# Performance work log

Hardware: AMD Instinct MI355X
Metric: run time of the kernel (lower is better)

## Reference

```python
import jax, jax.numpy as jnp
import numpy as np

NUM_STEPS = 8
THRESHOLD = 0.5


def _glorot(key, shape):
    fan_in = shape[0]
    return jax.random.normal(key, shape, dtype=jnp.float32) / np.sqrt(fan_in).astype(np.float32)


def setup_inputs() -> dict:
    key = jax.random.key(0)
    ks = jax.random.split(key, 24)
    B, APM = 2048, 32           # molecules, atoms per molecule
    N = B * APM                 # 65536 nodes
    E = N * 4                   # 262144 directed edges
    NF, EF, NH, EH, MA = 64, 16, 128, 128, 256
    inp = {}
    inp['mol_a_reprs'] = jax.random.normal(ks[0], (B, MA), dtype=jnp.float32)
    inp['node_features'] = jax.random.normal(ks[1], (N, NF), dtype=jnp.float32)
    inp['edge_features'] = jax.random.normal(ks[2], (E, EF), dtype=jnp.float32)
    inp['node_hidden0'] = jnp.zeros((N, NH), dtype=jnp.float32)
    inp['edge_hidden0'] = jnp.zeros((E, EH), dtype=jnp.float32)
    inp['edges'] = jax.random.randint(ks[3], (2, E), 0, N, dtype=jnp.int32)
    inp['batch_indices'] = jnp.repeat(jnp.arange(B, dtype=jnp.int32), APM)  # sorted, in-range
    # MPN weights (no bias)
    inp['W1'] = _glorot(ks[4], (NF, EH))   # src node features -> edge hidden
    inp['W2'] = _glorot(ks[5], (EF, EH))   # edge features -> edge hidden
    inp['W3'] = _glorot(ks[6], (NH, EH))   # src node hidden -> edge hidden
    inp['U1'] = _glorot(ks[7], (NF, NH))   # node features -> node hidden
    inp['U2'] = _glorot(ks[8], (EH, NH))   # aggregated edge hidden -> node hidden
    # pick-atom MLP: (MA+NH)->256->128->64->1
    inp['M1w'] = _glorot(ks[9], (MA + NH, 256)); inp['M1b'] = jnp.zeros((256,), jnp.float32)
    inp['M2w'] = _glorot(ks[10], (256, 128));    inp['M2b'] = jnp.zeros((128,), jnp.float32)
    inp['M3w'] = _glorot(ks[11], (128, 64));     inp['M3b'] = jnp.zeros((64,), jnp.float32)
    inp['M4w'] = _glorot(ks[12], (64, 1));       inp['M4b'] = jnp.zeros((1,), jnp.float32)
    return inp


def _mpn(node_features, edge_features, node_h, edge_h, src, dst, W1, W2, W3, U1, U2):
    N = node_features.shape[0]
    W1x_src = node_features[src] @ W1          # [E, EH], loop-invariant
    W2e = edge_features @ W2                   # [E, EH], loop-invariant
    U1x = node_features @ U1                   # [N, NH], loop-invariant
    for _ in range(NUM_STEPS):
        agg = jax.ops.segment_sum(edge_h, dst, num_segments=N)   # [N, EH]
        node_h = jax.nn.relu(U1x + agg @ U2)                     # [N, NH]
        edge_h = jax.nn.relu(W1x_src + W2e + node_h[src] @ W3)   # [E, EH]
    return node_h


def reference(mol_a_reprs, node_features, edge_features, node_hidden0, edge_hidden0,
              edges, batch_indices, W1, W2, W3, U1, U2,
              M1w, M1b, M2w, M2b, M3w, M3b, M4w, M4b):
    src, dst = edges[0], edges[1]
    node_h = _mpn(node_features, edge_features, node_hidden0, edge_hidden0,
                  src, dst, W1, W2, W3, U1, U2)
    b_atom_mol_a = mol_a_reprs[batch_indices]                    # index_select gather [N, MA]
    x = jnp.concatenate([node_h, b_atom_mol_a], axis=1)          # [N, NH+MA]
    x = jax.nn.relu(x @ M1w + M1b)
    x = jax.nn.relu(x @ M2w + M2b)
    x = jax.nn.relu(x @ M3w + M3b)
    p = jax.nn.sigmoid(x @ M4w + M4b)                            # [N, 1]
    return p >= THRESHOLD
```

## Files before the change

kernel.cpp:

```cpp
#include <hip/hip_runtime.h>
#include <cstddef>

#define NF 64
#define EF 16
#define NH 128
#define EH 128
#define MA 256

static inline int ceil_div(int a, int b) { return (a + b - 1) / b; }

__global__ __launch_bounds__(256) void gemm128_kernel(
    const float* __restrict__ A, const float* __restrict__ Bw,
    float* __restrict__ C,
    const float* __restrict__ addR, const int* __restrict__ addIdx,
    const float* __restrict__ bias, const int* __restrict__ gatherA,
    int M, int K, int Nc, int doRelu)
{
    __shared__ float As[16][132];
    __shared__ float Bs[16][132];
    const int tid = threadIdx.x;
    const int tx = tid & 15;
    const int ty = tid >> 4;
    const int m0 = blockIdx.y << 7;
    const int n0 = blockIdx.x << 7;

    const int lr = tid >> 1;
    const int lc = (tid & 1) << 3;
    const int br = tid >> 4;
    const int bc = (tid & 15) << 3;

    float acc[8][8];
#pragma unroll
    for (int i = 0; i < 8; ++i)
#pragma unroll
        for (int j = 0; j < 8; ++j) acc[i][j] = 0.0f;

    int arow = gatherA ? gatherA[m0 + lr] : (m0 + lr);
    const float* aptr = A + (size_t)arow * K + lc;

    for (int k0 = 0; k0 < K; k0 += 16) {
        float4 a0 = *(const float4*)(aptr + k0);
        float4 a1 = *(const float4*)(aptr + k0 + 4);
        float4 b0 = *(const float4*)(Bw + (size_t)(k0 + br) * Nc + n0 + bc);
        float4 b1 = *(const float4*)(Bw + (size_t)(k0 + br) * Nc + n0 + bc + 4);
        __syncthreads();
        As[lc + 0][lr] = a0.x; As[lc + 1][lr] = a0.y; As[lc + 2][lr] = a0.z; As[lc + 3][lr] = a0.w;
        As[lc + 4][lr] = a1.x; As[lc + 5][lr] = a1.y; As[lc + 6][lr] = a1.z; As[lc + 7][lr] = a1.w;
        *(float4*)&Bs[br][bc] = b0;
        *(float4*)&Bs[br][bc + 4] = b1;
        __syncthreads();
#pragma unroll
        for (int kk = 0; kk < 16; ++kk) {
            float4 av0 = *(const float4*)&As[kk][ty * 8];
            float4 av1 = *(const float4*)&As[kk][ty * 8 + 4];
            float4 bv0 = *(const float4*)&Bs[kk][tx * 8];
            float4 bv1 = *(const float4*)&Bs[kk][tx * 8 + 4];
            float a[8] = {av0.x, av0.y, av0.z, av0.w, av1.x, av1.y, av1.z, av1.w};
            float b[8] = {bv0.x, bv0.y, bv0.z, bv0.w, bv1.x, bv1.y, bv1.z, bv1.w};
#pragma unroll
            for (int i = 0; i < 8; ++i)
#pragma unroll
                for (int j = 0; j < 8; ++j)
                    acc[i][j] = fmaf(a[i], b[j], acc[i][j]);
        }
    }

    const int c = n0 + tx * 8;
    float4 bvl = make_float4(0.f, 0.f, 0.f, 0.f), bvh = bvl;
    if (bias) { bvl = *(const float4*)(bias + c); bvh = *(const float4*)(bias + c + 4); }
#pragma unroll
    for (int i = 0; i < 8; ++i) {
        int r = m0 + ty * 8 + i;
        float4 vl = make_float4(acc[i][0], acc[i][1], acc[i][2], acc[i][3]);
        float4 vh = make_float4(acc[i][4], acc[i][5], acc[i][6], acc[i][7]);
        if (addR) {
            int ar = addIdx ? addIdx[r] : r;
            float4 al = *(const float4*)(addR + (size_t)ar * Nc + c);
            float4 ah = *(const float4*)(addR + (size_t)ar * Nc + c + 4);
            vl.x += al.x; vl.y += al.y; vl.z += al.z; vl.w += al.w;
            vh.x += ah.x; vh.y += ah.y; vh.z += ah.z; vh.w += ah.w;
        }
        vl.x += bvl.x; vl.y += bvl.y; vl.z += bvl.z; vl.w += bvl.w;
        vh.x += bvh.x; vh.y += bvh.y; vh.z += bvh.z; vh.w += bvh.w;
        if (doRelu) {
            vl.x = fmaxf(vl.x, 0.f); vl.y = fmaxf(vl.y, 0.f); vl.z = fmaxf(vl.z, 0.f); vl.w = fmaxf(vl.w, 0.f);
            vh.x = fmaxf(vh.x, 0.f); vh.y = fmaxf(vh.y, 0.f); vh.z = fmaxf(vh.z, 0.f); vh.w = fmaxf(vh.w, 0.f);
        }
        *(float4*)(C + (size_t)r * Nc + c) = vl;
        *(float4*)(C + (size_t)r * Nc + c + 4) = vh;
    }
}

__global__ __launch_bounds__(256) void gemm_kernel(
    const float* __restrict__ A, const float* __restrict__ Bw,
    float* __restrict__ C,
    const float* __restrict__ addR, const int* __restrict__ addIdx,
    const float* __restrict__ bias,
    int M, int K, int Nc, int doRelu)
{
    __shared__ float As[16][64];
    __shared__ float Bs[16][64];
    const int tid = threadIdx.x;
    const int tx = tid & 15, ty = tid >> 4;
    const int m0 = blockIdx.y << 6;
    const int n0 = blockIdx.x << 6;
    const int lr = tid >> 2;
    const int lc = (tid & 3) << 2;
    const int bkr = tid >> 4;
    const int bc = (tid & 15) << 2;

    float acc[4][4];
#pragma unroll
    for (int i = 0; i < 4; ++i)
#pragma unroll
        for (int j = 0; j < 4; ++j) acc[i][j] = 0.0f;

    for (int k0 = 0; k0 < K; k0 += 16) {
        float4 a4 = *(const float4*)(A + (size_t)(m0 + lr) * K + (k0 + lc));
        float4 b4 = *(const float4*)(Bw + (size_t)(k0 + bkr) * Nc + (n0 + bc));
        __syncthreads();
        As[lc + 0][lr] = a4.x;
        As[lc + 1][lr] = a4.y;
        As[lc + 2][lr] = a4.z;
        As[lc + 3][lr] = a4.w;
        *(float4*)&Bs[bkr][bc] = b4;
        __syncthreads();
#pragma unroll
        for (int kk = 0; kk < 16; ++kk) {
            float a0 = As[kk][ty * 4 + 0];
            float a1 = As[kk][ty * 4 + 1];
            float a2 = As[kk][ty * 4 + 2];
            float a3 = As[kk][ty * 4 + 3];
            float b0 = Bs[kk][tx * 4 + 0];
            float b1 = Bs[kk][tx * 4 + 1];
            float b2 = Bs[kk][tx * 4 + 2];
            float b3 = Bs[kk][tx * 4 + 3];
            acc[0][0] += a0 * b0; acc[0][1] += a0 * b1; acc[0][2] += a0 * b2; acc[0][3] += a0 * b3;
            acc[1][0] += a1 * b0; acc[1][1] += a1 * b1; acc[1][2] += a1 * b2; acc[1][3] += a1 * b3;
            acc[2][0] += a2 * b0; acc[2][1] += a2 * b1; acc[2][2] += a2 * b2; acc[2][3] += a2 * b3;
            acc[3][0] += a3 * b0; acc[3][1] += a3 * b1; acc[3][2] += a3 * b2; acc[3][3] += a3 * b3;
        }
    }

    const int c = n0 + tx * 4;
    float4 bv = make_float4(0.f, 0.f, 0.f, 0.f);
    if (bias) bv = *(const float4*)(bias + c);
#pragma unroll
    for (int i = 0; i < 4; ++i) {
        int r = m0 + ty * 4 + i;
        float4 v = make_float4(acc[i][0], acc[i][1], acc[i][2], acc[i][3]);
        if (addR) {
            int ar = addIdx ? addIdx[r] : r;
            float4 ad = *(const float4*)(addR + (size_t)ar * Nc + c);
            v.x += ad.x; v.y += ad.y; v.z += ad.z; v.w += ad.w;
        }
        v.x += bv.x; v.y += bv.y; v.z += bv.z; v.w += bv.w;
        if (doRelu) {
            v.x = fmaxf(v.x, 0.f); v.y = fmaxf(v.y, 0.f);
            v.z = fmaxf(v.z, 0.f); v.w = fmaxf(v.w, 0.f);
        }
        *(float4*)(C + (size_t)r * Nc + c) = v;
    }
}

__global__ __launch_bounds__(256) void hist_kernel(const int* __restrict__ dst, int* __restrict__ deg, int E) {
    int e = blockIdx.x * 256 + threadIdx.x;
    if (e < E) atomicAdd(&deg[dst[e]], 1);
}

__global__ __launch_bounds__(256) void scan_block_kernel(const int* __restrict__ deg, int* __restrict__ rp,
                                                         int* __restrict__ bsum) {
    __shared__ int buf[256];
    int tid = threadIdx.x;
    int i = blockIdx.x * 256 + tid;
    int v = deg[i];
    buf[tid] = v;
    __syncthreads();
    for (int off = 1; off < 256; off <<= 1) {
        int t = (tid >= off) ? buf[tid - off] : 0;
        __syncthreads();
        buf[tid] += t;
        __syncthreads();
    }
    rp[i] = buf[tid] - v;
    if (tid == 255) bsum[blockIdx.x] = buf[255];
}

__global__ __launch_bounds__(256) void scan_top_kernel(const int* __restrict__ bsum, int* __restrict__ boff,
                                                       int* __restrict__ rp, int N) {
    __shared__ int buf[256];
    int tid = threadIdx.x;
    int v = bsum[tid];
    buf[tid] = v;
    __syncthreads();
    for (int off = 1; off < 256; off <<= 1) {
        int t = (tid >= off) ? buf[tid - off] : 0;
        __syncthreads();
        buf[tid] += t;
        __syncthreads();
    }
    boff[tid] = buf[tid] - v;
    if (tid == 255) rp[N] = buf[255];
}

__global__ __launch_bounds__(256) void scan_add_kernel(int* __restrict__ rp, int* __restrict__ cursor,
                                                       const int* __restrict__ boff) {
    int tid = threadIdx.x;
    int i = blockIdx.x * 256 + tid;
    int v = rp[i] + boff[blockIdx.x];
    rp[i] = v;
    cursor[i] = v;
}

__global__ __launch_bounds__(256) void scatter_kernel(const int* __restrict__ dst, const int* __restrict__ src,
                                                      int* __restrict__ cursor,
                                                      int* __restrict__ eid, int* __restrict__ srcS, int E) {
    int e = blockIdx.x * 256 + threadIdx.x;
    if (e < E) {
        int p = atomicAdd(&cursor[dst[e]], 1);
        eid[p] = e;
        srcS[p] = src[e];
    }
}

__global__ __launch_bounds__(256) void relu_copy_kernel(const float* __restrict__ in, float* __restrict__ out, int n4) {
    int i = blockIdx.x * 256 + threadIdx.x;
    if (i < n4) {
        float4 v = ((const float4*)in)[i];
        v.x = fmaxf(v.x, 0.f); v.y = fmaxf(v.y, 0.f);
        v.z = fmaxf(v.z, 0.f); v.w = fmaxf(v.w, 0.f);
        ((float4*)out)[i] = v;
    }
}

__global__ __launch_bounds__(128) void agg_kernel(const float* __restrict__ nodeT, const float* __restrict__ W2eS,
                                                  const int* __restrict__ rp, const int* __restrict__ srcS,
                                                  float* __restrict__ agg) {
    int n = blockIdx.x * 4 + threadIdx.y;
    int c = threadIdx.x << 2;
    int p0 = rp[n], p1 = rp[n + 1];
    float4 s = make_float4(0.f, 0.f, 0.f, 0.f);
    for (int p = p0; p < p1; ++p) {
        int sn = srcS[p];
        float4 t = *(const float4*)(nodeT + (size_t)sn * EH + c);
        float4 w = *(const float4*)(W2eS + (size_t)p * EH + c);
        s.x += fmaxf(t.x + w.x, 0.f);
        s.y += fmaxf(t.y + w.y, 0.f);
        s.z += fmaxf(t.z + w.z, 0.f);
        s.w += fmaxf(t.w + w.w, 0.f);
    }
    *(float4*)(agg + (size_t)n * EH + c) = s;
}

__global__ __launch_bounds__(256) void final_kernel(const float* __restrict__ x3, const float* __restrict__ w,
                                                    const float* __restrict__ b, int* __restrict__ out, int Nn) {
    int g = blockIdx.x * 256 + threadIdx.x;
    int n = g >> 6;
    int lane = threadIdx.x & 63;
    if (n < Nn) {
        float v = x3[(size_t)n * 64 + lane] * w[lane];
#pragma unroll
        for (int off = 32; off > 0; off >>= 1) v += __shfl_xor(v, off, 64);
        if (lane == 0) out[n] = (v + b[0]) >= 0.f ? 1 : 0;
    }
}

extern "C" void kernel_launch(void* const* d_in, const int* in_sizes, int n_in,
                              void* d_out, int out_size, void* d_ws, size_t ws_size,
                              hipStream_t stream)
{
    const float* mol_a = (const float*)d_in[0];
    const float* nf    = (const float*)d_in[1];
    const float* ef    = (const float*)d_in[2];
    const int*   edges = (const int*)d_in[5];
    const int*   batch = (const int*)d_in[6];
    const float* W1  = (const float*)d_in[7];
    const float* W2  = (const float*)d_in[8];
    const float* W3  = (const float*)d_in[9];
    const float* U1  = (const float*)d_in[10];
    const float* U2  = (const float*)d_in[11];
    const float* M1w = (const float*)d_in[12];
    const float* M1b = (const float*)d_in[13];
    const float* M2w = (const float*)d_in[14];
    const float* M2b = (const float*)d_in[15];
    const float* M3w = (const float*)d_in[16];
    const float* M3b = (const float*)d_in[17];
    const float* M4w = (const float*)d_in[18];
    const float* M4b = (const float*)d_in[19];

    const int N = in_sizes[3] / NH;
    const int E = in_sizes[4] / EH;
    const int B = in_sizes[0] / MA;
    const int* srcp = edges;
    const int* dstp = edges + E;

    char* ws = (char*)d_ws;
    size_t off = 0;
    auto alloc = [&](size_t bytes) -> char* {
        char* p = ws + off;
        off = (off + bytes + 255) & ~(size_t)255;
        return p;
    };
    int* deg     = (int*)alloc((size_t)N * 4);
    int* rp      = (int*)alloc(((size_t)N + 1) * 4);
    int* cursor  = (int*)alloc((size_t)N * 4);
    int* bsum    = (int*)alloc(256 * 4);
    int* boff    = (int*)alloc(256 * 4);
    int* eid     = (int*)alloc((size_t)E * 4);
    int* srcS    = (int*)alloc((size_t)E * 4);
    float* nodePre = (float*)alloc((size_t)N * EH * 4);
    float* U1x     = (float*)alloc((size_t)N * NH * 4);
    float* node_h  = (float*)alloc((size_t)N * NH * 4);
    float* nodeT   = (float*)alloc((size_t)N * EH * 4);
    float* aggp    = (float*)alloc((size_t)N * EH * 4);
    float* molPart = (float*)alloc((size_t)B * 256 * 4);
    float* W2eS    = (float*)alloc((size_t)E * EH * 4);
    float* x1 = (float*)W2eS;
    float* x2 = nodeT;
    float* x3 = aggp;

    hipMemsetAsync(deg, 0, (size_t)N * 4, stream);
    hist_kernel<<<ceil_div(E, 256), 256, 0, stream>>>(dstp, deg, E);
    scan_block_kernel<<<N / 256, 256, 0, stream>>>(deg, rp, bsum);
    scan_top_kernel<<<1, 256, 0, stream>>>(bsum, boff, rp, N);
    scan_add_kernel<<<N / 256, 256, 0, stream>>>(rp, cursor, boff);
    scatter_kernel<<<ceil_div(E, 256), 256, 0, stream>>>(dstp, srcp, cursor, eid, srcS, E);

    gemm128_kernel<<<dim3(1, N / 128), 256, 0, stream>>>(nf, W1, nodePre, nullptr, nullptr, nullptr, nullptr, N, NF, EH, 0);
    gemm128_kernel<<<dim3(1, E / 128), 256, 0, stream>>>(ef, W2, W2eS, nullptr, nullptr, nullptr, eid, E, EF, EH, 0);
    gemm128_kernel<<<dim3(1, N / 128), 256, 0, stream>>>(nf, U1, U1x, nullptr, nullptr, nullptr, nullptr, N, NF, NH, 0);

    relu_copy_kernel<<<(N * NH / 4) / 256, 256, 0, stream>>>(U1x, node_h, N * NH / 4);

    for (int s = 0; s < 7; ++s) {
        gemm128_kernel<<<dim3(1, N / 128), 256, 0, stream>>>(node_h, W3, nodeT, nodePre, nullptr, nullptr, nullptr, N, NH, EH, 0);
        agg_kernel<<<N / 4, dim3(32, 4), 0, stream>>>(nodeT, W2eS, rp, srcS, aggp);
        gemm128_kernel<<<dim3(1, N / 128), 256, 0, stream>>>(aggp, U2, node_h, U1x, nullptr, nullptr, nullptr, N, EH, NH, 1);
    }

    gemm_kernel<<<dim3(256 / 64, B / 64), 256, 0, stream>>>(mol_a, M1w + 128 * 256, molPart, nullptr, nullptr, M1b, B, MA, 256, 0);
    gemm128_kernel<<<dim3(2, N / 128), 256, 0, stream>>>(node_h, M1w, x1, molPart, batch, nullptr, nullptr, N, NH, 256, 1);
    gemm128_kernel<<<dim3(1, N / 128), 256, 0, stream>>>(x1, M2w, x2, nullptr, nullptr, M2b, nullptr, N, 256, 128, 1);
    gemm_kernel<<<dim3(1, N / 64), 256, 0, stream>>>(x2, M3w, x3, nullptr, nullptr, M3b, N, 128, 64, 1);
    final_kernel<<<ceil_div(N * 64, 256), 256, 0, stream>>>(x3, M4w, M4b, (int*)d_out, N);
}
```

Baseline: 1.387 ms.

## Fuse aggregation, U2 and W3 GEMMs into one per-step kernel and fuse MLP tail

```diff
diff --git a/kernel.cpp b/kernel.cpp
--- a/kernel.cpp
+++ b/kernel.cpp
@@ -14,7 +14,7 @@
     float* __restrict__ C,
     const float* __restrict__ addR, const int* __restrict__ addIdx,
     const float* __restrict__ bias, const int* __restrict__ gatherA,
-    int M, int K, int Nc, int doRelu)
+    int M, int K, int Nc, int doRelu, int reluA)
 {
     __shared__ float As[16][132];
     __shared__ float Bs[16][132];
@@ -43,6 +43,10 @@
         float4 a1 = *(const float4*)(aptr + k0 + 4);
         float4 b0 = *(const float4*)(Bw + (size_t)(k0 + br) * Nc + n0 + bc);
         float4 b1 = *(const float4*)(Bw + (size_t)(k0 + br) * Nc + n0 + bc + 4);
+        if (reluA) {
+            a0.x = fmaxf(a0.x, 0.f); a0.y = fmaxf(a0.y, 0.f); a0.z = fmaxf(a0.z, 0.f); a0.w = fmaxf(a0.w, 0.f);
+            a1.x = fmaxf(a1.x, 0.f); a1.y = fmaxf(a1.y, 0.f); a1.z = fmaxf(a1.z, 0.f); a1.w = fmaxf(a1.w, 0.f);
+        }
         __syncthreads();
         As[lc + 0][lr] = a0.x; As[lc + 1][lr] = a0.y; As[lc + 2][lr] = a0.z; As[lc + 3][lr] = a0.w;
         As[lc + 4][lr] = a1.x; As[lc + 5][lr] = a1.y; As[lc + 6][lr] = a1.z; As[lc + 7][lr] = a1.w;
@@ -91,75 +95,131 @@
     }
 }
 
-__global__ __launch_bounds__(256) void gemm_kernel(
-    const float* __restrict__ A, const float* __restrict__ Bw,
-    float* __restrict__ C,
-    const float* __restrict__ addR, const int* __restrict__ addIdx,
-    const float* __restrict__ bias,
-    int M, int K, int Nc, int doRelu)
+__global__ __launch_bounds__(256, 2) void fused_step_kernel(
+    const float* __restrict__ nodeT_in, const float* __restrict__ W2eS,
+    const int* __restrict__ rp, const int* __restrict__ srcS,
+    const float* __restrict__ U1x, const float* __restrict__ U2,
+    const float* __restrict__ nodePre, const float* __restrict__ W3,
+    float* __restrict__ nodeT_out, float* __restrict__ node_h_out,
+    int writeNodeH, int doGemm2)
 {
-    __shared__ float As[16][64];
-    __shared__ float Bs[16][64];
+    __shared__ float As[128][132];
+    __shared__ float Bs[16][132];
     const int tid = threadIdx.x;
+    const int m0 = blockIdx.x << 7;
+
+    {
+        const int cx = (tid & 31) << 2;
+        const int ry = tid >> 5;
+        for (int rg = 0; rg < 16; ++rg) {
+            const int row = rg * 8 + ry;
+            const int n = m0 + row;
+            const int p0 = rp[n], p1 = rp[n + 1];
+            float4 s = make_float4(0.f, 0.f, 0.f, 0.f);
+            for (int p = p0; p < p1; ++p) {
+                const int sn = srcS[p];
+                float4 t = *(const float4*)(nodeT_in + (size_t)sn * EH + cx);
+                float4 w = *(const float4*)(W2eS + (size_t)p * EH + cx);
+                s.x += fmaxf(t.x + w.x, 0.f);
+                s.y += fmaxf(t.y + w.y, 0.f);
+                s.z += fmaxf(t.z + w.z, 0.f);
+                s.w += fmaxf(t.w + w.w, 0.f);
+            }
+            As[cx + 0][row] = s.x;
+            As[cx + 1][row] = s.y;
+            As[cx + 2][row] = s.z;
+            As[cx + 3][row] = s.w;
+        }
+    }
+    __syncthreads();
+
     const int tx = tid & 15, ty = tid >> 4;
-    const int m0 = blockIdx.y << 6;
-    const int n0 = blockIdx.x << 6;
-    const int lr = tid >> 2;
-    const int lc = (tid & 3) << 2;
-    const int bkr = tid >> 4;
-    const int bc = (tid & 15) << 2;
-
-    float acc[4][4];
-#pragma unroll
-    for (int i = 0; i < 4; ++i)
-#pragma unroll
-        for (int j = 0; j < 4; ++j) acc[i][j] = 0.0f;
-
-    for (int k0 = 0; k0 < K; k0 += 16) {
-        float4 a4 = *(const float4*)(A + (size_t)(m0 + lr) * K + (k0 + lc));
-        float4 b4 = *(const float4*)(Bw + (size_t)(k0 + bkr) * Nc + (n0 + bc));
-        __syncthreads();
-        As[lc + 0][lr] = a4.x;
-        As[lc + 1][lr] = a4.y;
-        As[lc + 2][lr] = a4.z;
-        As[lc + 3][lr] = a4.w;
-        *(float4*)&Bs[bkr][bc] = b4;
-        __syncthreads();
-#pragma unroll
-        for (int kk = 0; kk < 16; ++kk) {
-            float a0 = As[kk][ty * 4 + 0];
-            float a1 = As[kk][ty * 4 + 1];
-            float a2 = As[kk][ty * 4 + 2];
-            float a3 = As[kk][ty * 4 + 3];
-            float b0 = Bs[kk][tx * 4 + 0];
-            float b1 = Bs[kk][tx * 4 + 1];
-            float b2 = Bs[kk][tx * 4 + 2];
-            float b3 = Bs[kk][tx * 4 + 3];
-            acc[0][0] += a0 * b0; acc[0][1] += a0 * b1; acc[0][2] += a0 * b2; acc[0][3] += a0 * b3;
-            acc[1][0] += a1 * b0; acc[1][1] += a1 * b1; acc[1][2] += a1 * b2; acc[1][3] += a1 * b3;
-            acc[2][0] += a2 * b0; acc[2][1] += a2 * b1; acc[2][2] += a2 * b2; acc[2][3] += a2 * b3;
-            acc[3][0] += a3 * b0; acc[3][1] += a3 * b1; acc[3][2] += a3 * b2; acc[3][3] += a3 * b3;
-        }
-    }
-
-    const int c = n0 + tx * 4;
-    float4 bv = make_float4(0.f, 0.f, 0.f, 0.f);
-    if (bias) bv = *(const float4*)(bias + c);
-#pragma unroll
-    for (int i = 0; i < 4; ++i) {
-        int r = m0 + ty * 4 + i;
-        float4 v = make_float4(acc[i][0], acc[i][1], acc[i][2], acc[i][3]);
-        if (addR) {
-            int ar = addIdx ? addIdx[r] : r;
-            float4 ad = *(const float4*)(addR + (size_t)ar * Nc + c);
-            v.x += ad.x; v.y += ad.y; v.z += ad.z; v.w += ad.w;
-        }
-        v.x += bv.x; v.y += bv.y; v.z += bv.z; v.w += bv.w;
-        if (doRelu) {
-            v.x = fmaxf(v.x, 0.f); v.y = fmaxf(v.y, 0.f);
-            v.z = fmaxf(v.z, 0.f); v.w = fmaxf(v.w, 0.f);
-        }
-        *(float4*)(C + (size_t)r * Nc + c) = v;
+    const int br = tid >> 4, bc = (tid & 15) << 3;
+
+    float acc[8][8];
+#pragma unroll
+    for (int i = 0; i < 8; ++i)
+#pragma unroll
+        for (int j = 0; j < 8; ++j) acc[i][j] = 0.0f;
+
+#define FUSED_GEMM(WPTR)                                                          \
+    for (int k0 = 0; k0 < 128; k0 += 16) {                                        \
+        float4 b0 = *(const float4*)(WPTR + (size_t)(k0 + br) * 128 + bc);        \
+        float4 b1 = *(const float4*)(WPTR + (size_t)(k0 + br) * 128 + bc + 4);    \
+        __syncthreads();                                                          \
+        *(float4*)&Bs[br][bc] = b0;                                               \
+        *(float4*)&Bs[br][bc + 4] = b1;                                           \
+        __syncthreads();                                                          \
+        _Pragma("unroll")                                                         \
+        for (int kk = 0; kk < 16; ++kk) {                                         \
+            float4 av0 = *(const float4*)&As[k0 + kk][ty * 8];                    \
+            float4 av1 = *(const float4*)&As[k0 + kk][ty * 8 + 4];                \
+            float4 bv0 = *(const float4*)&Bs[kk][tx * 8];                         \
+            float4 bv1 = *(const float4*)&Bs[kk][tx * 8 + 4];                     \
+            float a[8] = {av0.x, av0.y, av0.z, av0.w, av1.x, av1.y, av1.z, av1.w};\
+            float b[8] = {bv0.x, bv0.y, bv0.z, bv0.w, bv1.x, bv1.y, bv1.z, bv1.w};\
+            _Pragma("unroll")                                                     \
+            for (int i = 0; i < 8; ++i)                                           \
+                _Pragma("unroll")                                                 \
+                for (int j = 0; j < 8; ++j)                                       \
+                    acc[i][j] = fmaf(a[i], b[j], acc[i][j]);                      \
+        }                                                                         \
+    }
+
+    FUSED_GEMM(U2)
+
+    const int c = tx * 8;
+#pragma unroll
+    for (int i = 0; i < 8; ++i) {
+        const int r = m0 + ty * 8 + i;
+        float4 u0 = *(const float4*)(U1x + (size_t)r * NH + c);
+        float4 u1 = *(const float4*)(U1x + (size_t)r * NH + c + 4);
+        acc[i][0] = fmaxf(acc[i][0] + u0.x, 0.f);
+        acc[i][1] = fmaxf(acc[i][1] + u0.y, 0.f);
+        acc[i][2] = fmaxf(acc[i][2] + u0.z, 0.f);
+        acc[i][3] = fmaxf(acc[i][3] + u0.w, 0.f);
+        acc[i][4] = fmaxf(acc[i][4] + u1.x, 0.f);
+        acc[i][5] = fmaxf(acc[i][5] + u1.y, 0.f);
+        acc[i][6] = fmaxf(acc[i][6] + u1.z, 0.f);
+        acc[i][7] = fmaxf(acc[i][7] + u1.w, 0.f);
+    }
+    if (writeNodeH) {
+#pragma unroll
+        for (int i = 0; i < 8; ++i) {
+            const int r = m0 + ty * 8 + i;
+            *(float4*)(node_h_out + (size_t)r * NH + c) =
+                make_float4(acc[i][0], acc[i][1], acc[i][2], acc[i][3]);
+            *(float4*)(node_h_out + (size_t)r * NH + c + 4) =
+                make_float4(acc[i][4], acc[i][5], acc[i][6], acc[i][7]);
+        }
+    }
+    if (!doGemm2) return;
+
+    __syncthreads();
+#pragma unroll
+    for (int i = 0; i < 8; ++i)
+#pragma unroll
+        for (int j = 0; j < 8; ++j)
+            As[tx * 8 + j][ty * 8 + i] = acc[i][j];
+    __syncthreads();
+
+#pragma unroll
+    for (int i = 0; i < 8; ++i)
+#pragma unroll
+        for (int j = 0; j < 8; ++j) acc[i][j] = 0.0f;
+
+    FUSED_GEMM(W3)
+#undef FUSED_GEMM
+
+#pragma unroll
+    for (int i = 0; i < 8; ++i) {
+        const int r = m0 + ty * 8 + i;
+        float4 p0 = *(const float4*)(nodePre + (size_t)r * EH + c);
+        float4 p1 = *(const float4*)(nodePre + (size_t)r * EH + c + 4);
+        *(float4*)(nodeT_out + (size_t)r * EH + c) =
+            make_float4(acc[i][0] + p0.x, acc[i][1] + p0.y, acc[i][2] + p0.z, acc[i][3] + p0.w);
+        *(float4*)(nodeT_out + (size_t)r * EH + c + 4) =
+            make_float4(acc[i][4] + p1.x, acc[i][5] + p1.y, acc[i][6] + p1.z, acc[i][7] + p1.w);
     }
 }
 
@@ -223,45 +283,67 @@
     }
 }
 
-__global__ __launch_bounds__(256) void relu_copy_kernel(const float* __restrict__ in, float* __restrict__ out, int n4) {
-    int i = blockIdx.x * 256 + threadIdx.x;
-    if (i < n4) {
-        float4 v = ((const float4*)in)[i];
-        v.x = fmaxf(v.x, 0.f); v.y = fmaxf(v.y, 0.f);
-        v.z = fmaxf(v.z, 0.f); v.w = fmaxf(v.w, 0.f);
-        ((float4*)out)[i] = v;
-    }
-}
-
-__global__ __launch_bounds__(128) void agg_kernel(const float* __restrict__ nodeT, const float* __restrict__ W2eS,
-                                                  const int* __restrict__ rp, const int* __restrict__ srcS,
-                                                  float* __restrict__ agg) {
-    int n = blockIdx.x * 4 + threadIdx.y;
-    int c = threadIdx.x << 2;
-    int p0 = rp[n], p1 = rp[n + 1];
-    float4 s = make_float4(0.f, 0.f, 0.f, 0.f);
-    for (int p = p0; p < p1; ++p) {
-        int sn = srcS[p];
-        float4 t = *(const float4*)(nodeT + (size_t)sn * EH + c);
-        float4 w = *(const float4*)(W2eS + (size_t)p * EH + c);
-        s.x += fmaxf(t.x + w.x, 0.f);
-        s.y += fmaxf(t.y + w.y, 0.f);
-        s.z += fmaxf(t.z + w.z, 0.f);
-        s.w += fmaxf(t.w + w.w, 0.f);
-    }
-    *(float4*)(agg + (size_t)n * EH + c) = s;
-}
-
-__global__ __launch_bounds__(256) void final_kernel(const float* __restrict__ x3, const float* __restrict__ w,
-                                                    const float* __restrict__ b, int* __restrict__ out, int Nn) {
-    int g = blockIdx.x * 256 + threadIdx.x;
-    int n = g >> 6;
-    int lane = threadIdx.x & 63;
-    if (n < Nn) {
-        float v = x3[(size_t)n * 64 + lane] * w[lane];
-#pragma unroll
-        for (int off = 32; off > 0; off >>= 1) v += __shfl_xor(v, off, 64);
-        if (lane == 0) out[n] = (v + b[0]) >= 0.f ? 1 : 0;
+__global__ __launch_bounds__(256) void x3final_kernel(const float* __restrict__ x2, const float* __restrict__ M3w,
+                                                      const float* __restrict__ b3, const float* __restrict__ M4w,
+                                                      const float* __restrict__ b4, int* __restrict__ out) {
+    __shared__ float As[16][132];
+    __shared__ float Bs[16][68];
+    __shared__ float red[128][17];
+    const int tid = threadIdx.x;
+    const int tx = tid & 15;
+    const int ty = tid >> 4;
+    const int m0 = blockIdx.x << 7;
+    const int lr = tid >> 1, lc = (tid & 1) << 3;
+    const int br = tid >> 4, bc = (tid & 15) << 2;
+
+    float acc[8][4];
+#pragma unroll
+    for (int i = 0; i < 8; ++i)
+#pragma unroll
+        for (int j = 0; j < 4; ++j) acc[i][j] = 0.0f;
+
+    const float* aptr = x2 + (size_t)(m0 + lr) * 128 + lc;
+    for (int k0 = 0; k0 < 128; k0 += 16) {
+        float4 a0 = *(const float4*)(aptr + k0);
+        float4 a1 = *(const float4*)(aptr + k0 + 4);
+        float4 bv = *(const float4*)(M3w + (size_t)(k0 + br) * 64 + bc);
+        __syncthreads();
+        As[lc + 0][lr] = a0.x; As[lc + 1][lr] = a0.y; As[lc + 2][lr] = a0.z; As[lc + 3][lr] = a0.w;
+        As[lc + 4][lr] = a1.x; As[lc + 5][lr] = a1.y; As[lc + 6][lr] = a1.z; As[lc + 7][lr] = a1.w;
+        *(float4*)&Bs[br][bc] = bv;
+        __syncthreads();
+#pragma unroll
+        for (int kk = 0; kk < 16; ++kk) {
+            float4 av0 = *(const float4*)&As[kk][ty * 8];
+            float4 av1 = *(const float4*)&As[kk][ty * 8 + 4];
+            float4 bv0 = *(const float4*)&Bs[kk][tx * 4];
+            float a[8] = {av0.x, av0.y, av0.z, av0.w, av1.x, av1.y, av1.z, av1.w};
+            float b[4] = {bv0.x, bv0.y, bv0.z, bv0.w};
+#pragma unroll
+            for (int i = 0; i < 8; ++i)
+#pragma unroll
+                for (int j = 0; j < 4; ++j)
+                    acc[i][j] = fmaf(a[i], b[j], acc[i][j]);
+        }
+    }
+
+    const int c = tx * 4;
+    float4 b3v = *(const float4*)(b3 + c);
+    float4 w4v = *(const float4*)(M4w + c);
+#pragma unroll
+    for (int i = 0; i < 8; ++i) {
+        float p = fmaxf(acc[i][0] + b3v.x, 0.f) * w4v.x
+                + fmaxf(acc[i][1] + b3v.y, 0.f) * w4v.y
+                + fmaxf(acc[i][2] + b3v.z, 0.f) * w4v.z
+                + fmaxf(acc[i][3] + b3v.w, 0.f) * w4v.w;
+        red[ty * 8 + i][tx] = p;
+    }
+    __syncthreads();
+    if (tid < 128) {
+        float z = b4[0];
+#pragma unroll
+        for (int j = 0; j < 16; ++j) z += red[tid][j];
+        out[m0 + tid] = z >= 0.f ? 1 : 0;
     }
 }
 
@@ -311,13 +393,12 @@
     float* nodePre = (float*)alloc((size_t)N * EH * 4);
     float* U1x     = (float*)alloc((size_t)N * NH * 4);
     float* node_h  = (float*)alloc((size_t)N * NH * 4);
-    float* nodeT   = (float*)alloc((size_t)N * EH * 4);
-    float* aggp    = (float*)alloc((size_t)N * EH * 4);
+    float* nodeTa  = (float*)alloc((size_t)N * EH * 4);
+    float* nodeTb  = (float*)alloc((size_t)N * EH * 4);
     float* molPart = (float*)alloc((size_t)B * 256 * 4);
     float* W2eS    = (float*)alloc((size_t)E * EH * 4);
     float* x1 = (float*)W2eS;
-    float* x2 = nodeT;
-    float* x3 = aggp;
+    float* x2 = nodeTa;
 
     hipMemsetAsync(deg, 0, (size_t)N * 4, stream);
     hist_kernel<<<ceil_div(E, 256), 256, 0, stream>>>(dstp, deg, E);
@@ -326,21 +407,24 @@
     scan_add_kernel<<<N / 256, 256, 0, stream>>>(rp, cursor, boff);
     scatter_kernel<<<ceil_div(E, 256), 256, 0, stream>>>(dstp, srcp, cursor, eid, srcS, E);
 
-    gemm128_kernel<<<dim3(1, N / 128), 256, 0, stream>>>(nf, W1, nodePre, nullptr, nullptr, nullptr, nullptr, N, NF, EH, 0);
-    gemm128_kernel<<<dim3(1, E / 128), 256, 0, stream>>>(ef, W2, W2eS, nullptr, nullptr, nullptr, eid, E, EF, EH, 0);
-    gemm128_kernel<<<dim3(1, N / 128), 256, 0, stream>>>(nf, U1, U1x, nullptr, nullptr, nullptr, nullptr, N, NF, NH, 0);
-
-    relu_copy_kernel<<<(N * NH / 4) / 256, 256, 0, stream>>>(U1x, node_h, N * NH / 4);
-
-    for (int s = 0; s < 7; ++s) {
-        gemm128_kernel<<<dim3(1, N / 128), 256, 0, stream>>>(node_h, W3, nodeT, nodePre, nullptr, nullptr, nullptr, N, NH, EH, 0);
-        agg_kernel<<<N / 4, dim3(32, 4), 0, stream>>>(nodeT, W2eS, rp, srcS, aggp);
-        gemm128_kernel<<<dim3(1, N / 128), 256, 0, stream>>>(aggp, U2, node_h, U1x, nullptr, nullptr, nullptr, N, EH, NH, 1);
-    }
-
-    gemm_kernel<<<dim3(256 / 64, B / 64), 256, 0, stream>>>(mol_a, M1w + 128 * 256, molPart, nullptr, nullptr, M1b, B, MA, 256, 0);
-    gemm128_kernel<<<dim3(2, N / 128), 256, 0, stream>>>(node_h, M1w, x1, molPart, batch, nullptr, nullptr, N, NH, 256, 1);
-    gemm128_kernel<<<dim3(1, N / 128), 256, 0, stream>>>(x1, M2w, x2, nullptr, nullptr, M2b, nullptr, N, 256, 128, 1);
-    gemm_kernel<<<dim3(1, N / 64), 256, 0, stream>>>(x2, M3w, x3, nullptr, nullptr, M3b, N, 128, 64, 1);
-    final_kernel<<<ceil_div(N * 64, 256), 256, 0, stream>>>(x3, M4w, M4b, (int*)d_out, N);
-}
+    gemm128_kernel<<<dim3(1, N / 128), 256, 0, stream>>>(nf, W1, nodePre, nullptr, nullptr, nullptr, nullptr, N, NF, EH, 0, 0);
+    gemm128_kernel<<<dim3(1, E / 128), 256, 0, stream>>>(ef, W2, W2eS, nullptr, nullptr, nullptr, eid, E, EF, EH, 0, 0);
+    gemm128_kernel<<<dim3(1, N / 128), 256, 0, stream>>>(nf, U1, U1x, nullptr, nullptr, nullptr, nullptr, N, NF, NH, 0, 0);
+
+    gemm128_kernel<<<dim3(1, N / 128), 256, 0, stream>>>(U1x, W3, nodeTa, nodePre, nullptr, nullptr, nullptr, N, NH, EH, 0, 1);
+
+    float* curT = nodeTa;
+    float* nxtT = nodeTb;
+    for (int s = 0; s < 6; ++s) {
+        fused_step_kernel<<<N / 128, 256, 0, stream>>>(curT, W2eS, rp, srcS, U1x, U2, nodePre, W3,
+                                                       nxtT, nullptr, 0, 1);
+        float* t = curT; curT = nxtT; nxtT = t;
+    }
+    fused_step_kernel<<<N / 128, 256, 0, stream>>>(curT, W2eS, rp, srcS, U1x, U2, nodePre, W3,
+                                                   nxtT, node_h, 1, 0);
+
+    gemm128_kernel<<<dim3(2, B / 128), 256, 0, stream>>>(mol_a, M1w + 128 * 256, molPart, nullptr, nullptr, M1b, nullptr, B, MA, 256, 0, 0);
+    gemm128_kernel<<<dim3(2, N / 128), 256, 0, stream>>>(node_h, M1w, x1, molPart, batch, nullptr, nullptr, N, NH, 256, 1, 0);
+    gemm128_kernel<<<dim3(1, N / 128), 256, 0, stream>>>(x1, M2w, x2, nullptr, nullptr, M2b, nullptr, N, 256, 128, 1, 0);
+    x3final_kernel<<<N / 128, 256, 0, stream>>>(x2, M3w, M3b, M4w, M4b, (int*)d_out);
+}
```

Result: slower. 1.448 ms (+4.4%).
